# Kernel tuning notes

Hardware: AMD Instinct MI355X
Metric: run time of the kernel (lower is better)

The kernel has to match this reference:

```python
import jax, jax.numpy as jnp
import numpy as np

IN_DIM = 128
OUT_DIM = 128
DEGREE = 3
BATCH = 8192


def setup_inputs() -> dict:
    key = jax.random.key(0)
    k1, k2 = jax.random.split(key)
    x = jax.random.normal(k1, (BATCH, IN_DIM), dtype=jnp.float32)
    # coeff ~ 0.1*randn, shape [out_dim*in_dim, degree+1]
    coeff = 0.1 * jax.random.normal(k2, (OUT_DIM * IN_DIM, DEGREE + 1), dtype=jnp.float32)
    return {"x": x, "coeff": coeff}


def reference(x, coeff):
    # x: [B, in_dim], coeff: [out_dim*in_dim, D+1]
    # Original tiles x to [out_dim*in_dim, B]; edge i = (o*in_dim + j) uses x[:, j].
    # out[i,b] = sum_d coeff[i,d] * x[b, i % in_dim]**d, then sum over in_dim.
    B, in_dim = x.shape
    D1 = coeff.shape[-1]
    out_dim = coeff.shape[0] // in_dim
    exps = jnp.arange(D1, dtype=x.dtype)
    powed = x[:, :, None] ** exps            # [B, in_dim, D+1]
    c = coeff.reshape(out_dim, in_dim, D1)    # [out_dim, in_dim, D+1]
    # per-edge polynomial eval fused with sum over in_dim
    y = jnp.einsum('bid,oid->bo', powed, c)   # [B, out_dim]
    return y
```

## Files before the change

### kernel.cpp

```cpp
#include <hip/hip_runtime.h>


#define BATCH   8192
#define IN_DIM  128
#define OUT_DIM 128
#define KDIM    512
#define M_BLK   64
#define N_BLK   32
#define BK      128
#define NSTAGE  (KDIM / BK)
#define WPAD    520
#define APAD    136

typedef __attribute__((ext_vector_type(8))) short bf16x8;
typedef __attribute__((ext_vector_type(4))) float f32x4;

__device__ inline unsigned short f2bf(float f) {
    union { float f; unsigned int u; } v; v.f = f;
    unsigned int u = v.u;
    u += 0x7FFFu + ((u >> 16) & 1u);
    return (unsigned short)(u >> 16);
}

#if defined(__has_builtin)
#if __has_builtin(__builtin_amdgcn_cvt_pk_bf16_f32)
#define HAVE_HW_PKBF16 1
#endif
#endif

#ifdef HAVE_HW_PKBF16
typedef __attribute__((ext_vector_type(2))) __bf16 bf16x2_t;
__device__ inline unsigned int pk2(float a, float b) {
    bf16x2_t r = __builtin_amdgcn_cvt_pk_bf16_f32(a, b);
    union { bf16x2_t v; unsigned int u; } c; c.v = r; return c.u;
}
#else
__device__ inline unsigned int pk2(float a, float b) {
    return (unsigned int)f2bf(a) | ((unsigned int)f2bf(b) << 16);
}
#endif

__device__ inline void write_pow4(unsigned short* dst, const float4 v) {
    unsigned int o[8];
    o[0] = pk2(1.0f, v.x); o[1] = pk2(v.x * v.x, v.x * v.x * v.x);
    o[2] = pk2(1.0f, v.y); o[3] = pk2(v.y * v.y, v.y * v.y * v.y);
    o[4] = pk2(1.0f, v.z); o[5] = pk2(v.z * v.z, v.z * v.z * v.z);
    o[6] = pk2(1.0f, v.w); o[7] = pk2(v.w * v.w, v.w * v.w * v.w);
    *(uint4*)(dst)     = *(uint4*)&o[0];
    *(uint4*)(dst + 8) = *(uint4*)&o[4];
}

__global__ __launch_bounds__(256) void kan_mfma(const float* __restrict__ x,
                                                const float* __restrict__ coeff,
                                                float* __restrict__ out) {
    __shared__ __align__(16) unsigned short W_lds[N_BLK * WPAD];
    __shared__ __align__(16) unsigned short A_lds[2][M_BLK * APAD];

    const int t    = threadIdx.x;
    const int w    = t >> 6;
    const int lane = t & 63;
    const int q    = lane >> 4;
    const int r    = lane & 15;
    const int m0   = blockIdx.x * M_BLK;
    const int n0   = blockIdx.y * N_BLK;

    #pragma unroll
    for (int i = 0; i < 16; ++i) {
        const int f    = i * 256 + t;
        const int row  = f >> 7;
        const int col4 = f & 127;
        const float4 c = *(const float4*)&coeff[(size_t)(n0 + row) * KDIM + col4 * 4];
        uint2 o;
        o.x = pk2(c.x, c.y);
        o.y = pk2(c.z, c.w);
        *(uint2*)&W_lds[row * WPAD + col4 * 4] = o;
    }

    const int xr0 = t >> 3;
    const int xr1 = (t + 256) >> 3;
    const int xc4 = t & 7;

    float4 p0 = *(const float4*)&x[(size_t)(m0 + xr0) * IN_DIM + xc4 * 4];
    float4 p1 = *(const float4*)&x[(size_t)(m0 + xr1) * IN_DIM + xc4 * 4];
    write_pow4(&A_lds[0][xr0 * APAD + xc4 * 16], p0);
    write_pow4(&A_lds[0][xr1 * APAD + xc4 * 16], p1);
    __syncthreads();

    f32x4 acc0 = {0.f, 0.f, 0.f, 0.f};
    f32x4 acc1 = {0.f, 0.f, 0.f, 0.f};

    for (int s = 0; s < NSTAGE; ++s) {
        if (s + 1 < NSTAGE) {
            const int jc = (s + 1) * 32;
            p0 = *(const float4*)&x[(size_t)(m0 + xr0) * IN_DIM + jc + xc4 * 4];
            p1 = *(const float4*)&x[(size_t)(m0 + xr1) * IN_DIM + jc + xc4 * 4];
        }

        const unsigned short* Ab = A_lds[s & 1];
        #pragma unroll
        for (int u = 0; u < BK / 32; ++u) {
            const int ko = u * 32 + q * 8;
            const bf16x8 av = *(const bf16x8*)&Ab[(w * 16 + r) * APAD + ko];
            const bf16x8 b0 = *(const bf16x8*)&W_lds[r        * WPAD + s * BK + ko];
            const bf16x8 b1 = *(const bf16x8*)&W_lds[(16 + r) * WPAD + s * BK + ko];
            acc0 = __builtin_amdgcn_mfma_f32_16x16x32_bf16(av, b0, acc0, 0, 0, 0);
            acc1 = __builtin_amdgcn_mfma_f32_16x16x32_bf16(av, b1, acc1, 0, 0, 0);
        }

        if (s + 1 < NSTAGE) {
            unsigned short* An = A_lds[(s + 1) & 1];
            write_pow4(&An[xr0 * APAD + xc4 * 16], p0);
            write_pow4(&An[xr1 * APAD + xc4 * 16], p1);
            __syncthreads();
        }
    }

    float* obase = out + (size_t)(m0 + w * 16 + q * 4) * OUT_DIM + n0 + r;
    #pragma unroll
    for (int rr = 0; rr < 4; ++rr) {
        obase[rr * OUT_DIM]      = acc0[rr];
        obase[rr * OUT_DIM + 16] = acc1[rr];
    }
}

extern "C" void kernel_launch(void* const* d_in, const int* in_sizes, int n_in,
                              void* d_out, int out_size, void* d_ws, size_t ws_size,
                              hipStream_t stream) {
    const float* x     = (const float*)d_in[0];
    const float* coeff = (const float*)d_in[1];
    float* out = (float*)d_out;

    dim3 grid(BATCH / M_BLK, OUT_DIM / N_BLK);
    kan_mfma<<<grid, 256, 0, stream>>>(x, coeff, out);
}
```

Before: 60.91 us.

## Fold degree-0 terms into a per-output bias and shrink GEMM K to 384

```diff
diff --git a/kernel.cpp b/kernel.cpp
--- a/kernel.cpp
+++ b/kernel.cpp
@@ -5,12 +5,11 @@
 #define IN_DIM  128
 #define OUT_DIM 128
 #define KDIM    512
+#define KP      384
 #define M_BLK   64
 #define N_BLK   32
-#define BK      128
-#define NSTAGE  (KDIM / BK)
-#define WPAD    520
-#define APAD    136
+#define WPAD    392
+#define APAD    392
 
 typedef __attribute__((ext_vector_type(8))) short bf16x8;
 typedef __attribute__((ext_vector_type(4))) float f32x4;
@@ -40,21 +39,12 @@
 }
 #endif
 
-__device__ inline void write_pow4(unsigned short* dst, const float4 v) {
-    unsigned int o[8];
-    o[0] = pk2(1.0f, v.x); o[1] = pk2(v.x * v.x, v.x * v.x * v.x);
-    o[2] = pk2(1.0f, v.y); o[3] = pk2(v.y * v.y, v.y * v.y * v.y);
-    o[4] = pk2(1.0f, v.z); o[5] = pk2(v.z * v.z, v.z * v.z * v.z);
-    o[6] = pk2(1.0f, v.w); o[7] = pk2(v.w * v.w, v.w * v.w * v.w);
-    *(uint4*)(dst)     = *(uint4*)&o[0];
-    *(uint4*)(dst + 8) = *(uint4*)&o[4];
-}
-
-__global__ __launch_bounds__(256) void kan_mfma(const float* __restrict__ x,
-                                                const float* __restrict__ coeff,
-                                                float* __restrict__ out) {
+__global__ __launch_bounds__(256, 2) void kan_mfma(const float* __restrict__ x,
+                                                   const float* __restrict__ coeff,
+                                                   float* __restrict__ out) {
     __shared__ __align__(16) unsigned short W_lds[N_BLK * WPAD];
-    __shared__ __align__(16) unsigned short A_lds[2][M_BLK * APAD];
+    __shared__ __align__(16) unsigned short A_lds[M_BLK * APAD];
+    __shared__ float bias_lds[N_BLK];
 
     const int t    = threadIdx.x;
     const int w    = t >> 6;
@@ -64,62 +54,74 @@
     const int m0   = blockIdx.x * M_BLK;
     const int n0   = blockIdx.y * N_BLK;
 
-    #pragma unroll
-    for (int i = 0; i < 16; ++i) {
-        const int f    = i * 256 + t;
-        const int row  = f >> 7;
-        const int col4 = f & 127;
-        const float4 c = *(const float4*)&coeff[(size_t)(n0 + row) * KDIM + col4 * 4];
-        uint2 o;
-        o.x = pk2(c.x, c.y);
-        o.y = pk2(c.z, c.w);
-        *(uint2*)&W_lds[row * WPAD + col4 * 4] = o;
+    {
+        const int jl = lane * 2;
+        #pragma unroll
+        for (int i = 0; i < 8; ++i) {
+            const int row = i * 4 + w;
+            const float* cp = &coeff[(size_t)(n0 + row) * KDIM + (size_t)jl * 4];
+            const float4 cA = *(const float4*)cp;
+            const float4 cB = *(const float4*)(cp + 4);
+            unsigned short* Wr = &W_lds[row * WPAD + jl];
+            *(unsigned int*)(Wr)       = pk2(cA.y, cB.y);
+            *(unsigned int*)(Wr + 128) = pk2(cA.z, cB.z);
+            *(unsigned int*)(Wr + 256) = pk2(cA.w, cB.w);
+        }
     }
 
-    const int xr0 = t >> 3;
-    const int xr1 = (t + 256) >> 3;
-    const int xc4 = t & 7;
+    {
+        const int o = w * 8 + (lane >> 3);
+        const float* cp = &coeff[(size_t)(n0 + o) * KDIM + (size_t)(lane & 7) * 64];
+        float bsum = 0.f;
+        #pragma unroll
+        for (int jj = 0; jj < 16; ++jj) bsum += cp[jj * 4];
+        bsum += __shfl_xor(bsum, 1);
+        bsum += __shfl_xor(bsum, 2);
+        bsum += __shfl_xor(bsum, 4);
+        if ((lane & 7) == 0) bias_lds[o] = bsum;
+    }
 
-    float4 p0 = *(const float4*)&x[(size_t)(m0 + xr0) * IN_DIM + xc4 * 4];
-    float4 p1 = *(const float4*)&x[(size_t)(m0 + xr1) * IN_DIM + xc4 * 4];
-    write_pow4(&A_lds[0][xr0 * APAD + xc4 * 16], p0);
-    write_pow4(&A_lds[0][xr1 * APAD + xc4 * 16], p1);
+    #pragma unroll
+    for (int i = 0; i < 8; ++i) {
+        const int f   = i * 256 + t;
+        const int row = f >> 5;
+        const int c4  = f & 31;
+        const float4 v = *(const float4*)&x[(size_t)(m0 + row) * IN_DIM + c4 * 4];
+        const float x2a = v.x * v.x, x2b = v.y * v.y;
+        const float x2c = v.z * v.z, x2d = v.w * v.w;
+        uint2 s1, s2, s3;
+        s1.x = pk2(v.x, v.y);         s1.y = pk2(v.z, v.w);
+        s2.x = pk2(x2a, x2b);         s2.y = pk2(x2c, x2d);
+        s3.x = pk2(x2a * v.x, x2b * v.y); s3.y = pk2(x2c * v.z, x2d * v.w);
+        unsigned short* Ar = &A_lds[row * APAD + c4 * 4];
+        *(uint2*)(Ar)       = s1;
+        *(uint2*)(Ar + 128) = s2;
+        *(uint2*)(Ar + 256) = s3;
+    }
+
     __syncthreads();
 
     f32x4 acc0 = {0.f, 0.f, 0.f, 0.f};
     f32x4 acc1 = {0.f, 0.f, 0.f, 0.f};
-
-    for (int s = 0; s < NSTAGE; ++s) {
-        if (s + 1 < NSTAGE) {
-            const int jc = (s + 1) * 32;
-            p0 = *(const float4*)&x[(size_t)(m0 + xr0) * IN_DIM + jc + xc4 * 4];
-            p1 = *(const float4*)&x[(size_t)(m0 + xr1) * IN_DIM + jc + xc4 * 4];
-        }
-
-        const unsigned short* Ab = A_lds[s & 1];
-        #pragma unroll
-        for (int u = 0; u < BK / 32; ++u) {
-            const int ko = u * 32 + q * 8;
-            const bf16x8 av = *(const bf16x8*)&Ab[(w * 16 + r) * APAD + ko];
-            const bf16x8 b0 = *(const bf16x8*)&W_lds[r        * WPAD + s * BK + ko];
-            const bf16x8 b1 = *(const bf16x8*)&W_lds[(16 + r) * WPAD + s * BK + ko];
-            acc0 = __builtin_amdgcn_mfma_f32_16x16x32_bf16(av, b0, acc0, 0, 0, 0);
-            acc1 = __builtin_amdgcn_mfma_f32_16x16x32_bf16(av, b1, acc1, 0, 0, 0);
-        }
-
-        if (s + 1 < NSTAGE) {
-            unsigned short* An = A_lds[(s + 1) & 1];
-            write_pow4(&An[xr0 * APAD + xc4 * 16], p0);
-            write_pow4(&An[xr1 * APAD + xc4 * 16], p1);
-            __syncthreads();
-        }
+    const unsigned short* Ap = &A_lds[(w * 16 + r) * APAD + q * 8];
+    const unsigned short* B0 = &W_lds[r        * WPAD + q * 8];
+    const unsigned short* B1 = &W_lds[(16 + r) * WPAD + q * 8];
+    #pragma unroll
+    for (int u = 0; u < 12; ++u) {
+        const bf16x8 av = *(const bf16x8*)(Ap + u * 32);
+        const bf16x8 b0 = *(const bf16x8*)(B0 + u * 32);
+        const bf16x8 b1 = *(const bf16x8*)(B1 + u * 32);
+        acc0 = __builtin_amdgcn_mfma_f32_16x16x32_bf16(av, b0, acc0, 0, 0, 0);
+        acc1 = __builtin_amdgcn_mfma_f32_16x16x32_bf16(av, b1, acc1, 0, 0, 0);
     }
 
+    const float bb0 = bias_lds[r];
+    const float bb1 = bias_lds[16 + r];
     float* obase = out + (size_t)(m0 + w * 16 + q * 4) * OUT_DIM + n0 + r;
     #pragma unroll
     for (int rr = 0; rr < 4; ++rr) {
-        obase[rr * OUT_DIM]      = acc0[rr];
-        obase[rr * OUT_DIM + 16] = acc1[rr];
+        obase[rr * OUT_DIM]      = acc0[rr] + bb0;
+        obase[rr * OUT_DIM + 16] = acc1[rr] + bb1;
     }
 }
 
```

After: 63.50 us. +4.3%, slower.
